# Optimization experiments

Measured on AMD Instinct MI355X. Metric: run time of the kernel, lower is better.

## Reference

```python
import jax, jax.numpy as jnp
import numpy as np

B = 131072
EPS = 1e-5

def _attn(x, Wq, Wk, Wv, Wo):
    # x: (B, 10, 1); Wq/Wk/Wv: (1, 16); Wo: (16, 1)
    Q = x @ Wq  # (B, 10, 16)
    K = x @ Wk
    V = x @ Wv
    A = jnp.einsum('bqd,bkd->bqk', Q, K) / 4.0  # sqrt(16) = 4
    A = jax.nn.softmax(A, axis=1)  # NOTE: torch Softmax(dim=1) -> axis 1, not -1
    out = jnp.einsum('bqk,bkd->bqd', A, V) @ Wo  # (B, 10, 1)
    return out[..., 0]  # squeeze -> (B, 10)

def _bn(h, gamma, beta):
    # BatchNorm1d training-mode math (batch stats, biased variance)
    mu = jnp.mean(h, axis=0)
    var = jnp.mean(jnp.square(h - mu), axis=0)
    return gamma * (h - mu) * jax.lax.rsqrt(var + EPS) + beta

def setup_inputs() -> dict:
    key = jax.random.key(0)
    ks = jax.random.split(key, 24)
    n = lambda k, shp, s=1.0: (jax.random.normal(k, shp, dtype=jnp.float32) * s)
    inp = {
        'x':   n(ks[0], (B, 10, 1)),
        'Wq1': n(ks[1], (1, 16)), 'Wk1': n(ks[2], (1, 16)),
        'Wv1': n(ks[3], (1, 16)), 'Wo1': n(ks[4], (16, 1)),
        'Wq2': n(ks[5], (1, 16)), 'Wk2': n(ks[6], (1, 16)),
        'Wv2': n(ks[7], (1, 16)), 'Wo2': n(ks[8], (16, 1)),
        # layer1: Linear(10,128) BN ReLU Linear(128,256) BN ReLU Linear(256,10)
        'W1a': n(ks[9], (10, 128), 0.3), 'b1a': jnp.zeros((128,), jnp.float32),
        'g1a': jnp.ones((128,), jnp.float32), 'be1a': jnp.zeros((128,), jnp.float32),
        'W1b': n(ks[10], (128, 256), 0.09), 'b1b': jnp.zeros((256,), jnp.float32),
        'g1b': jnp.ones((256,), jnp.float32), 'be1b': jnp.zeros((256,), jnp.float32),
        'W1c': n(ks[11], (256, 10), 0.06), 'b1c': jnp.zeros((10,), jnp.float32),
        # layer2: Linear(10,128) BN ReLU Linear(128,256) BN ReLU Linear(256,2)
        'W2a': n(ks[12], (10, 128), 0.3), 'b2a': jnp.zeros((128,), jnp.float32),
        'g2a': jnp.ones((128,), jnp.float32), 'be2a': jnp.zeros((128,), jnp.float32),
        'W2b': n(ks[13], (128, 256), 0.09), 'b2b': jnp.zeros((256,), jnp.float32),
        'g2b': jnp.ones((256,), jnp.float32), 'be2b': jnp.zeros((256,), jnp.float32),
        'W2c': n(ks[14], (256, 2), 0.06), 'b2c': jnp.zeros((2,), jnp.float32),
    }
    return inp

def reference(x, Wq1, Wk1, Wv1, Wo1, Wq2, Wk2, Wv2, Wo2,
              W1a, b1a, g1a, be1a, W1b, b1b, g1b, be1b, W1c, b1c,
              W2a, b2a, g2a, be2a, W2b, b2b, g2b, be2b, W2c, b2c):
    h = _attn(x, Wq1, Wk1, Wv1, Wo1)                 # (B, 10)
    h = jax.nn.relu(_bn(h @ W1a + b1a, g1a, be1a))   # (B, 128)
    h = jax.nn.relu(_bn(h @ W1b + b1b, g1b, be1b))   # (B, 256)
    h = h @ W1c + b1c                                # (B, 10)
    h = _attn(h[..., None], Wq2, Wk2, Wv2, Wo2)      # (B, 10)
    h = jax.nn.relu(_bn(h @ W2a + b2a, g2a, be2a))   # (B, 128)
    h = jax.nn.relu(_bn(h @ W2b + b2b, g2b, be2b))   # (B, 256)
    return h @ W2c + b2c                             # (B, 2)
```

## Files before the change

kernel.cpp:

```cpp
#include <hip/hip_runtime.h>
#include <hip/hip_bf16.h>

#define EPS 1e-5f
constexpr int BN = 131072;
constexpr int NBKT = 32;

typedef __attribute__((ext_vector_type(8))) short bf16x8;
typedef __attribute__((ext_vector_type(4))) float f32x4;

constexpr size_t OFF_H   = 0;
constexpr size_t OFF_HH  = OFF_H  + (size_t)BN*10;
constexpr size_t OFF_M1  = OFF_HH + (size_t)BN*10;
constexpr size_t OFF_S2  = OFF_M1 + 65;
constexpr size_t OFF_M3  = OFF_S2 + 512;
constexpr size_t OFF_S4  = OFF_M3 + 65;
constexpr size_t OFF_WA1 = OFF_S4 + 512;
constexpr size_t OFF_BA1 = OFF_WA1 + 1280;
constexpr size_t OFF_WA2 = OFF_BA1 + 128;
constexpr size_t OFF_BA2 = OFF_WA2 + 1280;
constexpr size_t OFF_SC2 = OFF_BA2 + 128;
constexpr size_t OFF_TC2 = OFF_SC2 + 256;
constexpr size_t OFF_SC4 = OFF_TC2 + 256;
constexpr size_t OFF_TC4 = OFF_SC4 + 256;
constexpr size_t OFF_WB1 = OFF_TC4 + 256;
constexpr size_t OFF_BB1 = OFF_WB1 + 32768;
constexpr size_t OFF_WB2 = OFF_BB1 + 256;
constexpr size_t OFF_BB2 = OFF_WB2 + 32768;
constexpr size_t OFF_P1  = OFF_BB2 + 256;
constexpr size_t OFF_P3  = OFF_P1 + 1024*65;
constexpr size_t OFF_S2B = OFF_P3 + 1024*65;
constexpr size_t OFF_S4B = OFF_S2B + (size_t)NBKT*512;
constexpr size_t OFF_WT1 = OFF_S4B + (size_t)NBKT*512;
constexpr size_t OFF_WT2 = OFF_WT1 + 16384;
constexpr size_t OFF_END = OFF_WT2 + 16384;
constexpr size_t OFF_Z_BYTES = ((OFF_END*4 + 255) & ~(size_t)255);
constexpr size_t WS_NEED = OFF_Z_BYTES + (size_t)256*BN*2;

__device__ __forceinline__ float wsum(float v){
  v += __shfl_down(v, 32);
  v += __shfl_down(v, 16);
  v += __shfl_down(v, 8);
  v += __shfl_down(v, 4);
  v += __shfl_down(v, 2);
  v += __shfl_down(v, 1);
  return v;
}

__device__ __forceinline__ unsigned pk_bf16(float a, float b){
  union { __hip_bfloat16 h[2]; unsigned u; } cv;
  cv.h[0] = __float2bfloat16(a);
  cv.h[1] = __float2bfloat16(b);
  return cv.u;
}

__device__ __forceinline__ unsigned short bf16_1(float a){
  union { __hip_bfloat16 h; unsigned short u; } cv;
  cv.h = __float2bfloat16(a);
  return cv.u;
}

__device__ __forceinline__ void attn10(const float* xr, float cqk, float cvo, float* y){
  #pragma unroll
  for (int q=0;q<10;q++) y[q] = 0.f;
  #pragma unroll
  for (int k=0;k<10;k++){
    float t = cqk * xr[k];
    float m = t*xr[0];
    #pragma unroll
    for (int q=1;q<10;q++) m = fmaxf(m, t*xr[q]);
    float ex[10]; float s = 0.f;
    #pragma unroll
    for (int q=0;q<10;q++){ ex[q] = __expf(t*xr[q]-m); s += ex[q]; }
    float f = xr[k]/s;
    #pragma unroll
    for (int q=0;q<10;q++) y[q] += ex[q]*f;
  }
  #pragma unroll
  for (int q=0;q<10;q++) y[q] *= cvo;
}

__device__ __forceinline__ void moments_block(const float* y, float (*red)[65],
                                              float* Pb, int t){
  int lane = t & 63, w = t >> 6;
  #pragma unroll
  for (int i=0;i<10;i++){
    float v = wsum(y[i]);
    if (lane==0) red[w][i] = v;
  }
  #pragma unroll
  for (int i=0;i<10;i++){
    #pragma unroll
    for (int j=i;j<10;j++){
      float v = wsum(y[i]*y[j]);
      if (lane==0) red[w][10 + 10*i - i*(i-1)/2 + (j-i)] = v;
    }
  }
  __syncthreads();
  if (t < 65)
    Pb[(size_t)blockIdx.x*65 + t] = red[0][t]+red[1][t]+red[2][t]+red[3][t];
}

__device__ __forceinline__ void moments10(const float* y, float* M, int lane){
  #pragma unroll
  for (int i=0;i<10;i++){
    float s = wsum(y[i]);
    if (lane==0) atomicAdd(&M[i], s);
  }
  #pragma unroll
  for (int i=0;i<10;i++){
    #pragma unroll
    for (int j=i;j<10;j++){
      int id = 10*i - i*(i-1)/2 + (j-i);
      float s = wsum(y[i]*y[j]);
      if (lane==0) atomicAdd(&M[10+id], s);
    }
  }
}

__global__ __launch_bounds__(256) void k_attn_in(
    const float* __restrict__ x,
    const float* __restrict__ Wq, const float* __restrict__ Wk,
    const float* __restrict__ Wv, const float* __restrict__ Wo,
    float* __restrict__ h, float* __restrict__ Pb){
  __shared__ float xs[256][11];
  __shared__ float red[4][65];
  int t = threadIdx.x;
  size_t base = (size_t)blockIdx.x*2560;
  for (int idx=t; idx<2560; idx+=256) xs[idx/10][idx%10] = x[base+idx];
  float cqk=0.f, cvo=0.f;
  #pragma unroll
  for (int d=0;d<16;d++){ cqk += Wq[d]*Wk[d]; cvo += Wv[d]*Wo[d]; }
  cqk *= 0.25f;
  __syncthreads();
  float xr[10];
  #pragma unroll
  for (int q=0;q<10;q++) xr[q] = xs[t][q];
  float y[10];
  attn10(xr, cqk, cvo, y);
  #pragma unroll
  for (int q=0;q<10;q++) xs[t][q] = y[q];
  moments_block(y, red, Pb, t);
  for (int idx=t; idx<2560; idx+=256) h[base+idx] = xs[idx/10][idx%10];
}

__global__ void k_fold10_part(const float* __restrict__ Pb, int npart,
                              const float* __restrict__ W,
                              const float* __restrict__ bv, const float* __restrict__ g,
                              const float* __restrict__ be,
                              float* __restrict__ WT, float* __restrict__ bo){
  __shared__ float part[65][8];
  __shared__ float sM[65];
  int t = threadIdx.x;
  if (t < 520){
    int c = t>>3, k = t&7;
    int n = npart>>3;
    float acc = 0.f;
    #pragma unroll 4
    for (int i=0;i<n;i++) acc += Pb[(size_t)(k*n+i)*65 + c];
    part[c][k] = acc;
  }
  __syncthreads();
  if (t < 65){
    float a = 0.f;
    #pragma unroll
    for (int k=0;k<8;k++) a += part[t][k];
    sM[t] = a;
  }
  __syncthreads();
  int j = t;
  if (j >= 128) return;
  const float invB = 1.f/(float)BN;
  float Eh[10];
  #pragma unroll
  for (int i=0;i<10;i++) Eh[i] = sM[i]*invB;
  float wj[10];
  #pragma unroll
  for (int i=0;i<10;i++) wj[i] = W[i*128+j];
  float mu = bv[j];
  #pragma unroll
  for (int i=0;i<10;i++) mu += Eh[i]*wj[i];
  float var = 0.f;
  #pragma unroll
  for (int i=0;i<10;i++){
    #pragma unroll
    for (int l=0;l<10;l++){
      int a = i<l ? i : l, c = i<l ? l : i;
      int id = 10*a - a*(a-1)/2 + (c-a);
      float cov = sM[10+id]*invB - Eh[i]*Eh[l];
      var += wj[i]*wj[l]*cov;
    }
  }
  float s = g[j]*rsqrtf(var + EPS);
  #pragma unroll
  for (int i=0;i<10;i++) WT[j*10+i] = wj[i]*s;
  bo[j] = (bv[j]-mu)*s + be[j];
}

__global__ void k_fold10_atomic(const float* __restrict__ M,
                                const float* __restrict__ W,
                                const float* __restrict__ bv, const float* __restrict__ g,
                                const float* __restrict__ be,
                                float* __restrict__ WT, float* __restrict__ bo){
  int j = threadIdx.x;
  if (j >= 128) return;
  const float invB = 1.f/(float)BN;
  float Eh[10];
  #pragma unroll
  for (int i=0;i<10;i++) Eh[i] = M[i]*invB;
  float wj[10];
  #pragma unroll
  for (int i=0;i<10;i++) wj[i] = W[i*128+j];
  float mu = bv[j];
  #pragma unroll
  for (int i=0;i<10;i++) mu += Eh[i]*wj[i];
  float var = 0.f;
  #pragma unroll
  for (int i=0;i<10;i++){
    #pragma unroll
    for (int l=0;l<10;l++){
      int a = i<l ? i : l, c = i<l ? l : i;
      int id = 10*a - a*(a-1)/2 + (c-a);
      float cov = M[10+id]*invB - Eh[i]*Eh[l];
      var += wj[i]*wj[l]*cov;
    }
  }
  float s = g[j]*rsqrtf(var + EPS);
  #pragma unroll
  for (int i=0;i<10;i++) WT[j*10+i] = wj[i]*s;
  bo[j] = (bv[j]-mu)*s + be[j];
}

__global__ void k_fold_affine(const float* __restrict__ stats,
                              const float* __restrict__ g,
                              const float* __restrict__ be,
                              float* __restrict__ s, float* __restrict__ tt){
  int j = threadIdx.x;
  if (j >= 256) return;
  float su = 0.f, sq = 0.f;
  #pragma unroll 4
  for (int k=0;k<NBKT;k++){
    su += stats[k*512 + j];
    sq += stats[k*512 + 256 + j];
  }
  const float invB = 1.f/(float)BN;
  float mu  = su*invB;
  float var = sq*invB - mu*mu;
  float sc = g[j]*rsqrtf(var + EPS);
  s[j]  = sc;
  tt[j] = be[j] - mu*sc;
}

__global__ __launch_bounds__(256) void k_prep_wt2(
    const float* __restrict__ W1, const float* __restrict__ W2,
    unsigned short* __restrict__ WT1, unsigned short* __restrict__ WT2){
  int g = blockIdx.x;
  const float* W = (g < 128) ? W1 : W2;
  unsigned short* WT = (g < 128) ? WT1 : WT2;
  int idx = (g & 127)*256 + threadIdx.x;
  int c = idx >> 7, k = idx & 127;
  WT[idx] = bf16_1(W[k*256 + c]);
}

__global__ __launch_bounds__(256) void k_layer_mfma(
    const float* __restrict__ h,
    const float* __restrict__ WaT,
    const float* __restrict__ ba,
    const unsigned short* __restrict__ WT,
    const float* __restrict__ bb,
    unsigned short* __restrict__ zt,
    float* __restrict__ stats)
{
  __shared__ unsigned short zs[256*72];
  __shared__ float hs[64][11];
  __shared__ float sWaT[1280];
  __shared__ float sstats[512];
  unsigned short* h1s = zs;
  int t = threadIdx.x;
  int lane = t & 63, w = t >> 6;
  int ci = lane & 15, g = lane >> 4;
  size_t row0 = (size_t)blockIdx.x * 64;

  bf16x8 bfr[4][4];
  #pragma unroll
  for (int nt=0; nt<4; nt++)
    #pragma unroll
    for (int kt=0; kt<4; kt++){
      union { uint4 u; bf16x8 v; } cv;
      cv.u = *(const uint4*)(WT + (size_t)(w*64 + nt*16 + ci)*128 + kt*32 + g*8);
      bfr[nt][kt] = cv.v;
    }

  for (int idx = t; idx < 640; idx += 256) hs[idx/10][idx%10] = h[row0*10 + idx];
  for (int idx = t; idx < 1280; idx += 256) sWaT[idx] = WaT[idx];
  __syncthreads();

  {
    int r = lane;
    int i0 = w * 32;
    float hr[10];
    #pragma unroll
    for (int l=0;l<10;l++) hr[l] = hs[r][l];
    #pragma unroll
    for (int j=0;j<4;j++){
      unsigned pk[4];
      #pragma unroll
      for (int q=0;q<4;q++){
        int i = i0 + j*8 + q*2;
        float v0 = ba[i], v1 = ba[i+1];
        #pragma unroll
        for (int l=0;l<10;l++){
          v0 = fmaf(hr[l], sWaT[i*10+l],     v0);
          v1 = fmaf(hr[l], sWaT[(i+1)*10+l], v1);
        }
        pk[q] = pk_bf16(fmaxf(v0,0.f), fmaxf(v1,0.f));
      }
      int byte = r*256 + (((i0 + j*8)*2) ^ ((r&7)<<4));
      *(uint4*)((char*)h1s + byte) = make_uint4(pk[0],pk[1],pk[2],pk[3]);
    }
  }
  __syncthreads();

  f32x4 acc[4][4];
  #pragma unroll
  for (int mt=0;mt<4;mt++)
    #pragma unroll
    for (int nt=0;nt<4;nt++)
      acc[mt][nt] = (f32x4){0.f,0.f,0.f,0.f};

  #pragma unroll
  for (int mt=0; mt<4; mt++){
    int r = mt*16 + ci;
    bf16x8 af[4];
    #pragma unroll
    for (int kt=0; kt<4; kt++){
      int byte = r*256 + ((kt*64 + g*16) ^ ((r&7)<<4));
      af[kt] = *(const bf16x8*)((const char*)h1s + byte);
    }
    #pragma unroll
    for (int nt=0; nt<4; nt++)
      #pragma unroll
      for (int kt=0; kt<4; kt++)
        acc[mt][nt] = __builtin_amdgcn_mfma_f32_16x16x32_bf16(
            af[kt], bfr[nt][kt], acc[mt][nt], 0, 0, 0);
  }

  float bbv[4];
  #pragma unroll
  for (int nt=0;nt<4;nt++) bbv[nt] = bb[w*64 + nt*16 + ci];
  float csum[4] = {0,0,0,0}, csq[4] = {0,0,0,0};
  #pragma unroll
  for (int mt=0; mt<4; mt++)
    #pragma unroll
    for (int nt=0; nt<4; nt++)
      #pragma unroll
      for (int j=0;j<4;j++){
        float zv = acc[mt][nt][j] + bbv[nt];
        acc[mt][nt][j] = zv;
        csum[nt] += zv;
        csq[nt]  += zv*zv;
      }
  #pragma unroll
  for (int nt=0; nt<4; nt++){
    float s1 = csum[nt], s2 = csq[nt];
    s1 += __shfl_down(s1, 32); s1 += __shfl_down(s1, 16);
    s2 += __shfl_down(s2, 32); s2 += __shfl_down(s2, 16);
    if (lane < 16){
      sstats[w*64 + nt*16 + ci]       = s1;
      sstats[256 + w*64 + nt*16 + ci] = s2;
    }
  }
  __syncthreads();
  int bkt = blockIdx.x & (NBKT-1);
  atomicAdd(&stats[bkt*512 + t], sstats[t]);
  atomicAdd(&stats[bkt*512 + 256 + t], sstats[256+t]);

  #pragma unroll
  for (int mt=0; mt<4; mt++)
    #pragma unroll
    for (int nt=0; nt<4; nt++){
      int c = w*64 + nt*16 + ci;
      int r0 = mt*16 + g*4;
      uint2 v;
      v.x = pk_bf16(acc[mt][nt][0], acc[mt][nt][1]);
      v.y = pk_bf16(acc[mt][nt][2], acc[mt][nt][3]);
      *(uint2*)&zs[c*72 + r0] = v;
    }
  __syncthreads();

  #pragma unroll
  for (int pass=0; pass<8; pass++){
    int c  = (t>>3) + pass*32;
    int rc = (t&7)*8;
    uint4 v = *(const uint4*)&zs[c*72 + rc];
    *(uint4*)(zt + (size_t)c*BN + row0 + rc) = v;
  }
}

__global__ __launch_bounds__(256) void k_consume_mid(
    const unsigned short* __restrict__ zt,
    const float* __restrict__ s_g, const float* __restrict__ t_g,
    const float* __restrict__ Wc,  const float* __restrict__ bc,
    const float* __restrict__ Wq, const float* __restrict__ Wk,
    const float* __restrict__ Wv, const float* __restrict__ Wo,
    float* __restrict__ hh, float* __restrict__ Pb){
  __shared__ __align__(16) unsigned short zs[64*256];
  __shared__ float sW[2560];
  __shared__ float ss[256], st[256];
  __shared__ float red[4][65];
  int t = threadIdx.x;
  for (int idx=t; idx<2560; idx+=256) sW[idx] = Wc[idx];
  ss[t] = s_g[t]; st[t] = t_g[t];
  size_t b0 = (size_t)blockIdx.x*256;

  float z3[10];
  #pragma unroll
  for (int l=0;l<10;l++) z3[l] = bc[l];

  int lane32 = t & 31, cl8 = t >> 5;
  for (int cc=0; cc<4; cc++){
    __syncthreads();
    #pragma unroll
    for (int pass=0; pass<8; pass++){
      int c_local = pass*8 + cl8;
      int c = cc*64 + c_local;
      uint4 v = *(const uint4*)(zt + (size_t)c*BN + b0 + lane32*8);
      *(uint4*)&zs[c_local*256 + lane32*8] = v;
    }
    __syncthreads();
    #pragma unroll 8
    for (int c_local=0; c_local<64; c_local++){
      int c = cc*64 + c_local;
      float f = __uint_as_float(((unsigned)zs[c_local*256 + t]) << 16);
      float h2 = fmaxf(fmaf(ss[c], f, st[c]), 0.f);
      #pragma unroll
      for (int l=0;l<10;l++) z3[l] = fmaf(h2, sW[c*10+l], z3[l]);
    }
  }

  float cqk=0.f, cvo=0.f;
  #pragma unroll
  for (int d=0;d<16;d++){ cqk += Wq[d]*Wk[d]; cvo += Wv[d]*Wo[d]; }
  cqk *= 0.25f;
  float y[10];
  attn10(z3, cqk, cvo, y);
  __syncthreads();
  float* hhs = (float*)zs;
  #pragma unroll
  for (int q=0;q<10;q++) hhs[t*10+q] = y[q];
  moments_block(y, red, Pb, t);
  for (int idx=t; idx<2560; idx+=256)
    hh[b0*10 + idx] = hhs[idx];
}

__global__ __launch_bounds__(256) void k_consume_out(
    const unsigned short* __restrict__ zt,
    const float* __restrict__ s_g, const float* __restrict__ t_g,
    const float* __restrict__ Wc,  const float* __restrict__ bc,
    float* __restrict__ out){
  __shared__ __align__(16) unsigned short zs[64*256];
  __shared__ float sW0[256], sW1[256], ss[256], st[256];
  int t = threadIdx.x;
  sW0[t] = Wc[t*2]; sW1[t] = Wc[t*2+1];
  ss[t] = s_g[t]; st[t] = t_g[t];
  size_t b0 = (size_t)blockIdx.x*256;
  float o0 = bc[0], o1 = bc[1];
  int lane32 = t & 31, cl8 = t >> 5;
  for (int cc=0; cc<4; cc++){
    __syncthreads();
    #pragma unroll
    for (int pass=0; pass<8; pass++){
      int c_local = pass*8 + cl8;
      int c = cc*64 + c_local;
      uint4 v = *(const uint4*)(zt + (size_t)c*BN + b0 + lane32*8);
      *(uint4*)&zs[c_local*256 + lane32*8] = v;
    }
    __syncthreads();
    #pragma unroll 8
    for (int c_local=0; c_local<64; c_local++){
      int c = cc*64 + c_local;
      float f = __uint_as_float(((unsigned)zs[c_local*256 + t]) << 16);
      float h5 = fmaxf(fmaf(ss[c], f, st[c]), 0.f);
      o0 = fmaf(h5, sW0[c], o0);
      o1 = fmaf(h5, sW1[c], o1);
    }
  }
  *(float2*)(out + (b0 + t)*2) = make_float2(o0, o1);
}

__global__ void k_fold_big(const float* __restrict__ stats,
                           const float* __restrict__ W,
                           const float* __restrict__ bv, const float* __restrict__ g,
                           const float* __restrict__ be,
                           float* __restrict__ Wf, float* __restrict__ bf){
  int j = blockIdx.x*256 + threadIdx.x;
  if (j >= 256) return;
  const float invB = 1.f/(float)BN;
  float mu  = stats[j]*invB;
  float var = stats[256+j]*invB - mu*mu;
  float s = g[j]*rsqrtf(var + EPS);
  bf[j] = (bv[j]-mu)*s + be[j];
  for (int i=0;i<128;i++) Wf[i*256+j] = W[i*256+j]*s;
}

__global__ __launch_bounds__(256) void k_mid(
    const float* __restrict__ h,
    const float* __restrict__ WaT, const float* __restrict__ ba,
    const float* __restrict__ Wb,  const float* __restrict__ bb,
    float* __restrict__ stats){
  int b = blockIdx.x*256 + threadIdx.x;
  if (b >= BN) return;
  float hr[10];
  #pragma unroll
  for (int l=0;l<10;l++) hr[l] = h[(size_t)b*10+l];
  int lane = threadIdx.x & 63;
  for (int jc=0;jc<4;jc++){
    float acc[64];
    #pragma unroll
    for (int j=0;j<64;j++) acc[j] = bb[jc*64+j];
    for (int i=0;i<128;i++){
      float h1 = ba[i];
      #pragma unroll
      for (int l=0;l<10;l++) h1 += hr[l]*WaT[i*10+l];
      h1 = fmaxf(h1, 0.f);
      const float* __restrict__ w = &Wb[i*256 + jc*64];
      #pragma unroll
      for (int j=0;j<64;j++) acc[j] += h1*w[j];
    }
    #pragma unroll
    for (int j=0;j<64;j++){
      float s1 = wsum(acc[j]);
      float s2 = wsum(acc[j]*acc[j]);
      if (lane==0){
        atomicAdd(&stats[jc*64+j], s1);
        atomicAdd(&stats[256+jc*64+j], s2);
      }
    }
  }
}

__global__ __launch_bounds__(256) void k_mid2(
    const float* __restrict__ h,
    const float* __restrict__ WaT, const float* __restrict__ ba,
    const float* __restrict__ Wbf, const float* __restrict__ bbf,
    const float* __restrict__ Wc,  const float* __restrict__ bc,
    const float* __restrict__ Wq, const float* __restrict__ Wk,
    const float* __restrict__ Wv, const float* __restrict__ Wo,
    float* __restrict__ hh, float* __restrict__ M){
  int b = blockIdx.x*256 + threadIdx.x;
  if (b >= BN) return;
  float hr[10];
  #pragma unroll
  for (int l=0;l<10;l++) hr[l] = h[(size_t)b*10+l];
  float z3[10];
  #pragma unroll
  for (int l=0;l<10;l++) z3[l] = bc[l];
  for (int jc=0;jc<4;jc++){
    float acc[64];
    #pragma unroll
    for (int j=0;j<64;j++) acc[j] = bbf[jc*64+j];
    for (int i=0;i<128;i++){
      float h1 = ba[i];
      #pragma unroll
      for (int l=0;l<10;l++) h1 += hr[l]*WaT[i*10+l];
      h1 = fmaxf(h1, 0.f);
      const float* __restrict__ w = &Wbf[i*256 + jc*64];
      #pragma unroll
      for (int j=0;j<64;j++) acc[j] += h1*w[j];
    }
    #pragma unroll
    for (int j=0;j<64;j++){
      float h2 = fmaxf(acc[j], 0.f);
      const float* __restrict__ wc = &Wc[(jc*64+j)*10];
      #pragma unroll
      for (int l=0;l<10;l++) z3[l] += h2*wc[l];
    }
  }
  float cqk=0.f, cvo=0.f;
  #pragma unroll
  for (int d=0;d<16;d++){ cqk += Wq[d]*Wk[d]; cvo += Wv[d]*Wo[d]; }
  cqk *= 0.25f;
  float y[10];
  attn10(z3, cqk, cvo, y);
  #pragma unroll
  for (int q=0;q<10;q++) hh[(size_t)b*10+q] = y[q];
  moments10(y, M, threadIdx.x & 63);
}

__global__ __launch_bounds__(256) void k_out(
    const float* __restrict__ h,
    const float* __restrict__ WaT, const float* __restrict__ ba,
    const float* __restrict__ Wbf, const float* __restrict__ bbf,
    const float* __restrict__ Wc,  const float* __restrict__ bc,
    float* __restrict__ out){
  int b = blockIdx.x*256 + threadIdx.x;
  if (b >= BN) return;
  float hr[10];
  #pragma unroll
  for (int l=0;l<10;l++) hr[l] = h[(size_t)b*10+l];
  float o0 = bc[0], o1 = bc[1];
  for (int jc=0;jc<4;jc++){
    float acc[64];
    #pragma unroll
    for (int j=0;j<64;j++) acc[j] = bbf[jc*64+j];
    for (int i=0;i<128;i++){
      float h4 = ba[i];
      #pragma unroll
      for (int l=0;l<10;l++) h4 += hr[l]*WaT[i*10+l];
      h4 = fmaxf(h4, 0.f);
      const float* __restrict__ w = &Wbf[i*256 + jc*64];
      #pragma unroll
      for (int j=0;j<64;j++) acc[j] += h4*w[j];
    }
    #pragma unroll
    for (int j=0;j<64;j++){
      float h5 = fmaxf(acc[j], 0.f);
      o0 += h5*Wc[(jc*64+j)*2];
      o1 += h5*Wc[(jc*64+j)*2+1];
    }
  }
  out[(size_t)b*2]   = o0;
  out[(size_t)b*2+1] = o1;
}

extern "C" void kernel_launch(void* const* d_in, const int* in_sizes, int n_in,
                              void* d_out, int out_size, void* d_ws, size_t ws_size,
                              hipStream_t stream){
  const float* x   = (const float*)d_in[0];
  const float* Wq1 = (const float*)d_in[1];
  const float* Wk1 = (const float*)d_in[2];
  const float* Wv1 = (const float*)d_in[3];
  const float* Wo1 = (const float*)d_in[4];
  const float* Wq2 = (const float*)d_in[5];
  const float* Wk2 = (const float*)d_in[6];
  const float* Wv2 = (const float*)d_in[7];
  const float* Wo2 = (const float*)d_in[8];
  const float* W1a = (const float*)d_in[9];  const float* b1a = (const float*)d_in[10];
  const float* g1a = (const float*)d_in[11]; const float* be1a= (const float*)d_in[12];
  const float* W1b = (const float*)d_in[13]; const float* b1b = (const float*)d_in[14];
  const float* g1b = (const float*)d_in[15]; const float* be1b= (const float*)d_in[16];
  const float* W1c = (const float*)d_in[17]; const float* b1c = (const float*)d_in[18];
  const float* W2a = (const float*)d_in[19]; const float* b2a = (const float*)d_in[20];
  const float* g2a = (const float*)d_in[21]; const float* be2a= (const float*)d_in[22];
  const float* W2b = (const float*)d_in[23]; const float* b2b = (const float*)d_in[24];
  const float* g2b = (const float*)d_in[25]; const float* be2b= (const float*)d_in[26];
  const float* W2c = (const float*)d_in[27]; const float* b2c = (const float*)d_in[28];

  float* f   = (float*)d_ws;
  float* h   = f + OFF_H;
  float* hh  = f + OFF_HH;
  float* M1  = f + OFF_M1;
  float* S2  = f + OFF_S2;
  float* M3  = f + OFF_M3;
  float* S4  = f + OFF_S4;
  float* WA1 = f + OFF_WA1; float* BA1 = f + OFF_BA1;
  float* WA2 = f + OFF_WA2; float* BA2 = f + OFF_BA2;
  float* SC2 = f + OFF_SC2; float* TC2 = f + OFF_TC2;
  float* SC4 = f + OFF_SC4; float* TC4 = f + OFF_TC4;
  float* WB1 = f + OFF_WB1; float* BB1 = f + OFF_BB1;
  float* WB2 = f + OFF_WB2; float* BB2 = f + OFF_BB2;
  float* P1  = f + OFF_P1;  float* P3  = f + OFF_P3;
  float* S2B = f + OFF_S2B; float* S4B = f + OFF_S4B;
  unsigned short* WT1 = (unsigned short*)(f + OFF_WT1);
  unsigned short* WT2 = (unsigned short*)(f + OFF_WT2);
  unsigned short* ZT = (unsigned short*)((char*)d_ws + OFF_Z_BYTES);

  dim3 blk(256);
  dim3 grid256(BN/256);
  dim3 grid64(BN/64);

  if (ws_size >= WS_NEED){
    hipMemsetAsync(S2B, 0, (size_t)2*NBKT*512*sizeof(float), stream);
    k_prep_wt2<<<256,blk,0,stream>>>(W1b, W2b, WT1, WT2);
    k_attn_in<<<grid256,blk,0,stream>>>(x, Wq1,Wk1,Wv1,Wo1, h, P1);
    k_fold10_part<<<1,576,0,stream>>>(P1, 512, W1a,b1a,g1a,be1a, WA1,BA1);
    k_layer_mfma<<<grid64,blk,0,stream>>>(h, WA1,BA1, WT1,b1b, ZT, S2B);
    k_fold_affine<<<1,256,0,stream>>>(S2B, g1b, be1b, SC2, TC2);
    k_consume_mid<<<grid256,blk,0,stream>>>(ZT, SC2,TC2, W1c,b1c,
                                            Wq2,Wk2,Wv2,Wo2, hh, P3);
    k_fold10_part<<<1,576,0,stream>>>(P3, 512, W2a,b2a,g2a,be2a, WA2,BA2);
    k_layer_mfma<<<grid64,blk,0,stream>>>(hh, WA2,BA2, WT2,b2b, ZT, S4B);
    k_fold_affine<<<1,256,0,stream>>>(S4B, g2b, be2b, SC4, TC4);
    k_consume_out<<<grid256,blk,0,stream>>>(ZT, SC4,TC4, W2c,b2c, (float*)d_out);
  } else {
    hipMemsetAsync(M1, 0, (65+512+65+512)*sizeof(float), stream);
    k_attn_in<<<grid256,blk,0,stream>>>(x, Wq1,Wk1,Wv1,Wo1, h, P1);
    k_fold10_part<<<1,576,0,stream>>>(P1, 512, W1a,b1a,g1a,be1a, WA1,BA1);
    k_mid<<<grid256,blk,0,stream>>>(h, WA1,BA1, W1b,b1b, S2);
    k_fold_big<<<1,256,0,stream>>>(S2, W1b,b1b,g1b,be1b, WB1,BB1);
    k_mid2<<<grid256,blk,0,stream>>>(h, WA1,BA1, WB1,BB1, W1c,b1c,
                                     Wq2,Wk2,Wv2,Wo2, hh, M3);
    k_fold10_atomic<<<1,128,0,stream>>>(M3, W2a,b2a,g2a,be2a, WA2,BA2);
    k_mid<<<grid256,blk,0,stream>>>(hh, WA2,BA2, W2b,b2b, S4);
    k_fold_big<<<1,256,0,stream>>>(S4, W2b,b2b,g2b,be2b, WB2,BB2);
    k_out<<<grid256,blk,0,stream>>>(hh, WA2,BA2, WB2,BB2, W2c,b2c, (float*)d_out);
  }
}
```

Measured before the change: 209.9 us.

## Recompute 128x256 GEMM instead of materializing bf16 activations to HBM

```diff
diff --git a/kernel.cpp b/kernel.cpp
--- a/kernel.cpp
+++ b/kernel.cpp
@@ -27,14 +27,13 @@
 constexpr size_t OFF_WB2 = OFF_BB1 + 256;
 constexpr size_t OFF_BB2 = OFF_WB2 + 32768;
 constexpr size_t OFF_P1  = OFF_BB2 + 256;
-constexpr size_t OFF_P3  = OFF_P1 + 1024*65;
-constexpr size_t OFF_S2B = OFF_P3 + 1024*65;
+constexpr size_t OFF_P3  = OFF_P1 + 2048*65;
+constexpr size_t OFF_S2B = OFF_P3 + 2048*65;
 constexpr size_t OFF_S4B = OFF_S2B + (size_t)NBKT*512;
 constexpr size_t OFF_WT1 = OFF_S4B + (size_t)NBKT*512;
 constexpr size_t OFF_WT2 = OFF_WT1 + 16384;
 constexpr size_t OFF_END = OFF_WT2 + 16384;
-constexpr size_t OFF_Z_BYTES = ((OFF_END*4 + 255) & ~(size_t)255);
-constexpr size_t WS_NEED = OFF_Z_BYTES + (size_t)256*BN*2;
+constexpr size_t WS_NEED = OFF_END*4;
 
 __device__ __forceinline__ float wsum(float v){
   v += __shfl_down(v, 32);
@@ -231,6 +230,7 @@
 }
 
 __global__ void k_fold_affine(const float* __restrict__ stats,
+                              const float* __restrict__ bb,
                               const float* __restrict__ g,
                               const float* __restrict__ be,
                               float* __restrict__ s, float* __restrict__ tt){
@@ -247,7 +247,7 @@
   float var = sq*invB - mu*mu;
   float sc = g[j]*rsqrtf(var + EPS);
   s[j]  = sc;
-  tt[j] = be[j] - mu*sc;
+  tt[j] = be[j] - mu*sc + sc*bb[j];
 }
 
 __global__ __launch_bounds__(256) void k_prep_wt2(
@@ -261,24 +261,14 @@
   WT[idx] = bf16_1(W[k*256 + c]);
 }
 
-__global__ __launch_bounds__(256) void k_layer_mfma(
-    const float* __restrict__ h,
-    const float* __restrict__ WaT,
-    const float* __restrict__ ba,
-    const unsigned short* __restrict__ WT,
-    const float* __restrict__ bb,
-    unsigned short* __restrict__ zt,
-    float* __restrict__ stats)
+__device__ __forceinline__ void block_gemm(
+    const float* __restrict__ h, const float* __restrict__ WaT,
+    const float* __restrict__ ba, const unsigned short* __restrict__ WT,
+    unsigned short* h1s, float (*hs)[11], float* sWaT,
+    f32x4 (&acc)[4][4], int t, size_t row0)
 {
-  __shared__ unsigned short zs[256*72];
-  __shared__ float hs[64][11];
-  __shared__ float sWaT[1280];
-  __shared__ float sstats[512];
-  unsigned short* h1s = zs;
-  int t = threadIdx.x;
   int lane = t & 63, w = t >> 6;
   int ci = lane & 15, g = lane >> 4;
-  size_t row0 = (size_t)blockIdx.x * 64;
 
   bf16x8 bfr[4][4];
   #pragma unroll
@@ -320,7 +310,6 @@
   }
   __syncthreads();
 
-  f32x4 acc[4][4];
   #pragma unroll
   for (int mt=0;mt<4;mt++)
     #pragma unroll
@@ -343,6 +332,24 @@
         acc[mt][nt] = __builtin_amdgcn_mfma_f32_16x16x32_bf16(
             af[kt], bfr[nt][kt], acc[mt][nt], 0, 0, 0);
   }
+}
+
+__global__ __launch_bounds__(256) void k_stats(
+    const float* __restrict__ h, const float* __restrict__ WaT,
+    const float* __restrict__ ba, const unsigned short* __restrict__ WT,
+    const float* __restrict__ bb, float* __restrict__ stats)
+{
+  __shared__ unsigned short h1s[64*128];
+  __shared__ float hs[64][11];
+  __shared__ float sWaT[1280];
+  __shared__ float sstats[512];
+  int t = threadIdx.x;
+  int lane = t & 63, w = t >> 6;
+  int ci = lane & 15;
+  size_t row0 = (size_t)blockIdx.x * 64;
+
+  f32x4 acc[4][4];
+  block_gemm(h, WaT, ba, WT, h1s, hs, sWaT, acc, t, row0);
 
   float bbv[4];
   #pragma unroll
@@ -355,7 +362,6 @@
       #pragma unroll
       for (int j=0;j<4;j++){
         float zv = acc[mt][nt][j] + bbv[nt];
-        acc[mt][nt][j] = zv;
         csum[nt] += zv;
         csq[nt]  += zv*zv;
       }
@@ -373,118 +379,166 @@
   int bkt = blockIdx.x & (NBKT-1);
   atomicAdd(&stats[bkt*512 + t], sstats[t]);
   atomicAdd(&stats[bkt*512 + 256 + t], sstats[256+t]);
-
-  #pragma unroll
-  for (int mt=0; mt<4; mt++)
-    #pragma unroll
-    for (int nt=0; nt<4; nt++){
-      int c = w*64 + nt*16 + ci;
-      int r0 = mt*16 + g*4;
-      uint2 v;
-      v.x = pk_bf16(acc[mt][nt][0], acc[mt][nt][1]);
-      v.y = pk_bf16(acc[mt][nt][2], acc[mt][nt][3]);
-      *(uint2*)&zs[c*72 + r0] = v;
-    }
-  __syncthreads();
-
-  #pragma unroll
-  for (int pass=0; pass<8; pass++){
-    int c  = (t>>3) + pass*32;
-    int rc = (t&7)*8;
-    uint4 v = *(const uint4*)&zs[c*72 + rc];
-    *(uint4*)(zt + (size_t)c*BN + row0 + rc) = v;
-  }
-}
-
-__global__ __launch_bounds__(256) void k_consume_mid(
-    const unsigned short* __restrict__ zt,
+}
+
+__global__ __launch_bounds__(256) void k_fuse_mid(
+    const float* __restrict__ h, const float* __restrict__ WaT,
+    const float* __restrict__ ba, const unsigned short* __restrict__ WT,
     const float* __restrict__ s_g, const float* __restrict__ t_g,
     const float* __restrict__ Wc,  const float* __restrict__ bc,
     const float* __restrict__ Wq, const float* __restrict__ Wk,
     const float* __restrict__ Wv, const float* __restrict__ Wo,
-    float* __restrict__ hh, float* __restrict__ Pb){
-  __shared__ __align__(16) unsigned short zs[64*256];
-  __shared__ float sW[2560];
-  __shared__ float ss[256], st[256];
-  __shared__ float red[4][65];
+    float* __restrict__ hh, float* __restrict__ Pb)
+{
+  __shared__ unsigned short h1s[64*128];
+  __shared__ float hs[64][11];
+  __shared__ float sWaT[1280];
+  __shared__ float sWc[2560];
+  __shared__ float ssv[256], stv[256];
+  __shared__ float z3part[4][64][10];
+  __shared__ float red[65];
+  __shared__ float hhs[64][10];
   int t = threadIdx.x;
-  for (int idx=t; idx<2560; idx+=256) sW[idx] = Wc[idx];
-  ss[t] = s_g[t]; st[t] = t_g[t];
-  size_t b0 = (size_t)blockIdx.x*256;
-
-  float z3[10];
-  #pragma unroll
-  for (int l=0;l<10;l++) z3[l] = bc[l];
-
-  int lane32 = t & 31, cl8 = t >> 5;
-  for (int cc=0; cc<4; cc++){
-    __syncthreads();
-    #pragma unroll
-    for (int pass=0; pass<8; pass++){
-      int c_local = pass*8 + cl8;
-      int c = cc*64 + c_local;
-      uint4 v = *(const uint4*)(zt + (size_t)c*BN + b0 + lane32*8);
-      *(uint4*)&zs[c_local*256 + lane32*8] = v;
-    }
-    __syncthreads();
-    #pragma unroll 8
-    for (int c_local=0; c_local<64; c_local++){
-      int c = cc*64 + c_local;
-      float f = __uint_as_float(((unsigned)zs[c_local*256 + t]) << 16);
-      float h2 = fmaxf(fmaf(ss[c], f, st[c]), 0.f);
-      #pragma unroll
-      for (int l=0;l<10;l++) z3[l] = fmaf(h2, sW[c*10+l], z3[l]);
-    }
-  }
+  int lane = t & 63, w = t >> 6;
+  int ci = lane & 15, g = lane >> 4;
+  size_t row0 = (size_t)blockIdx.x * 64;
+
+  for (int idx=t; idx<2560; idx+=256) sWc[idx] = Wc[idx];
+  ssv[t] = s_g[t]; stv[t] = t_g[t];
+
+  f32x4 acc[4][4];
+  block_gemm(h, WaT, ba, WT, h1s, hs, sWaT, acc, t, row0);
+
+  float sv[4], tv[4], wcv[4][10];
+  #pragma unroll
+  for (int nt=0;nt<4;nt++){
+    int c = w*64 + nt*16 + ci;
+    sv[nt] = ssv[c]; tv[nt] = stv[c];
+    #pragma unroll
+    for (int l=0;l<10;l++) wcv[nt][l] = sWc[c*10+l];
+  }
+
+  #pragma unroll
+  for (int mt=0; mt<4; mt++){
+    #pragma unroll
+    for (int j=0;j<4;j++){
+      float p[10];
+      #pragma unroll
+      for (int l=0;l<10;l++) p[l] = 0.f;
+      #pragma unroll
+      for (int nt=0;nt<4;nt++){
+        float h2 = fmaxf(fmaf(sv[nt], acc[mt][nt][j], tv[nt]), 0.f);
+        #pragma unroll
+        for (int l=0;l<10;l++) p[l] = fmaf(h2, wcv[nt][l], p[l]);
+      }
+      #pragma unroll
+      for (int off=1; off<16; off<<=1){
+        #pragma unroll
+        for (int l=0;l<10;l++) p[l] += __shfl_xor(p[l], off);
+      }
+      if (ci==0){
+        int row = mt*16 + g*4 + j;
+        #pragma unroll
+        for (int l=0;l<10;l++) z3part[w][row][l] = p[l];
+      }
+    }
+  }
+  __syncthreads();
 
   float cqk=0.f, cvo=0.f;
   #pragma unroll
   for (int d=0;d<16;d++){ cqk += Wq[d]*Wk[d]; cvo += Wv[d]*Wo[d]; }
   cqk *= 0.25f;
+
   float y[10];
-  attn10(z3, cqk, cvo, y);
-  __syncthreads();
-  float* hhs = (float*)zs;
-  #pragma unroll
-  for (int q=0;q<10;q++) hhs[t*10+q] = y[q];
-  moments_block(y, red, Pb, t);
-  for (int idx=t; idx<2560; idx+=256)
-    hh[b0*10 + idx] = hhs[idx];
-}
-
-__global__ __launch_bounds__(256) void k_consume_out(
-    const unsigned short* __restrict__ zt,
+  if (t < 64){
+    float z3[10];
+    #pragma unroll
+    for (int l=0;l<10;l++)
+      z3[l] = bc[l] + z3part[0][t][l] + z3part[1][t][l]
+                    + z3part[2][t][l] + z3part[3][t][l];
+    attn10(z3, cqk, cvo, y);
+    #pragma unroll
+    for (int q=0;q<10;q++) hhs[t][q] = y[q];
+    #pragma unroll
+    for (int i=0;i<10;i++){
+      float v = wsum(y[i]);
+      if (lane==0) red[i] = v;
+    }
+    #pragma unroll
+    for (int i=0;i<10;i++){
+      #pragma unroll
+      for (int j=i;j<10;j++){
+        float v = wsum(y[i]*y[j]);
+        if (lane==0) red[10 + 10*i - i*(i-1)/2 + (j-i)] = v;
+      }
+    }
+  }
+  __syncthreads();
+  if (t < 65) Pb[(size_t)blockIdx.x*65 + t] = red[t];
+  const float* hhsf = (const float*)hhs;
+  for (int idx=t; idx<640; idx+=256) hh[row0*10 + idx] = hhsf[idx];
+}
+
+__global__ __launch_bounds__(256) void k_fuse_out(
+    const float* __restrict__ h, const float* __restrict__ WaT,
+    const float* __restrict__ ba, const unsigned short* __restrict__ WT,
     const float* __restrict__ s_g, const float* __restrict__ t_g,
     const float* __restrict__ Wc,  const float* __restrict__ bc,
-    float* __restrict__ out){
-  __shared__ __align__(16) unsigned short zs[64*256];
-  __shared__ float sW0[256], sW1[256], ss[256], st[256];
+    float* __restrict__ out)
+{
+  __shared__ unsigned short h1s[64*128];
+  __shared__ float hs[64][11];
+  __shared__ float sWaT[1280];
+  __shared__ float sW0[256], sW1[256], ssv[256], stv[256];
+  __shared__ float opart[4][64][2];
   int t = threadIdx.x;
+  int lane = t & 63, w = t >> 6;
+  int ci = lane & 15, g = lane >> 4;
+  size_t row0 = (size_t)blockIdx.x * 64;
+
   sW0[t] = Wc[t*2]; sW1[t] = Wc[t*2+1];
-  ss[t] = s_g[t]; st[t] = t_g[t];
-  size_t b0 = (size_t)blockIdx.x*256;
-  float o0 = bc[0], o1 = bc[1];
-  int lane32 = t & 31, cl8 = t >> 5;
-  for (int cc=0; cc<4; cc++){
-    __syncthreads();
-    #pragma unroll
-    for (int pass=0; pass<8; pass++){
-      int c_local = pass*8 + cl8;
-      int c = cc*64 + c_local;
-      uint4 v = *(const uint4*)(zt + (size_t)c*BN + b0 + lane32*8);
-      *(uint4*)&zs[c_local*256 + lane32*8] = v;
-    }
-    __syncthreads();
-    #pragma unroll 8
-    for (int c_local=0; c_local<64; c_local++){
-      int c = cc*64 + c_local;
-      float f = __uint_as_float(((unsigned)zs[c_local*256 + t]) << 16);
-      float h5 = fmaxf(fmaf(ss[c], f, st[c]), 0.f);
-      o0 = fmaf(h5, sW0[c], o0);
-      o1 = fmaf(h5, sW1[c], o1);
-    }
-  }
-  *(float2*)(out + (b0 + t)*2) = make_float2(o0, o1);
+  ssv[t] = s_g[t];  stv[t] = t_g[t];
+
+  f32x4 acc[4][4];
+  block_gemm(h, WaT, ba, WT, h1s, hs, sWaT, acc, t, row0);
+
+  float sv[4], tv[4], w0[4], w1[4];
+  #pragma unroll
+  for (int nt=0;nt<4;nt++){
+    int c = w*64 + nt*16 + ci;
+    sv[nt] = ssv[c]; tv[nt] = stv[c];
+    w0[nt] = sW0[c]; w1[nt] = sW1[c];
+  }
+  #pragma unroll
+  for (int mt=0; mt<4; mt++){
+    #pragma unroll
+    for (int j=0;j<4;j++){
+      float p0 = 0.f, p1 = 0.f;
+      #pragma unroll
+      for (int nt=0;nt<4;nt++){
+        float h5 = fmaxf(fmaf(sv[nt], acc[mt][nt][j], tv[nt]), 0.f);
+        p0 = fmaf(h5, w0[nt], p0);
+        p1 = fmaf(h5, w1[nt], p1);
+      }
+      #pragma unroll
+      for (int off=1; off<16; off<<=1){
+        p0 += __shfl_xor(p0, off);
+        p1 += __shfl_xor(p1, off);
+      }
+      if (ci==0){
+        int row = mt*16 + g*4 + j;
+        opart[w][row][0] = p0;
+        opart[w][row][1] = p1;
+      }
+    }
+  }
+  __syncthreads();
+  if (t < 64){
+    float o0 = bc[0] + opart[0][t][0]+opart[1][t][0]+opart[2][t][0]+opart[3][t][0];
+    float o1 = bc[1] + opart[0][t][1]+opart[1][t][1]+opart[2][t][1]+opart[3][t][1];
+    *(float2*)(out + (row0 + t)*2) = make_float2(o0, o1);
+  }
 }
 
 __global__ void k_fold_big(const float* __restrict__ stats,
@@ -662,7 +716,6 @@
   float* S2B = f + OFF_S2B; float* S4B = f + OFF_S4B;
   unsigned short* WT1 = (unsigned short*)(f + OFF_WT1);
   unsigned short* WT2 = (unsigned short*)(f + OFF_WT2);
-  unsigned short* ZT = (unsigned short*)((char*)d_ws + OFF_Z_BYTES);
 
   dim3 blk(256);
   dim3 grid256(BN/256);
@@ -673,14 +726,15 @@
     k_prep_wt2<<<256,blk,0,stream>>>(W1b, W2b, WT1, WT2);
     k_attn_in<<<grid256,blk,0,stream>>>(x, Wq1,Wk1,Wv1,Wo1, h, P1);
     k_fold10_part<<<1,576,0,stream>>>(P1, 512, W1a,b1a,g1a,be1a, WA1,BA1);
-    k_layer_mfma<<<grid64,blk,0,stream>>>(h, WA1,BA1, WT1,b1b, ZT, S2B);
-    k_fold_affine<<<1,256,0,stream>>>(S2B, g1b, be1b, SC2, TC2);
-    k_consume_mid<<<grid256,blk,0,stream>>>(ZT, SC2,TC2, W1c,b1c,
-                                            Wq2,Wk2,Wv2,Wo2, hh, P3);
-    k_fold10_part<<<1,576,0,stream>>>(P3, 512, W2a,b2a,g2a,be2a, WA2,BA2);
-    k_layer_mfma<<<grid64,blk,0,stream>>>(hh, WA2,BA2, WT2,b2b, ZT, S4B);
-    k_fold_affine<<<1,256,0,stream>>>(S4B, g2b, be2b, SC4, TC4);
-    k_consume_out<<<grid256,blk,0,stream>>>(ZT, SC4,TC4, W2c,b2c, (float*)d_out);
+    k_stats<<<grid64,blk,0,stream>>>(h, WA1,BA1, WT1, b1b, S2B);
+    k_fold_affine<<<1,256,0,stream>>>(S2B, b1b, g1b, be1b, SC2, TC2);
+    k_fuse_mid<<<grid64,blk,0,stream>>>(h, WA1,BA1, WT1, SC2,TC2, W1c,b1c,
+                                        Wq2,Wk2,Wv2,Wo2, hh, P3);
+    k_fold10_part<<<1,576,0,stream>>>(P3, 2048, W2a,b2a,g2a,be2a, WA2,BA2);
+    k_stats<<<grid64,blk,0,stream>>>(hh, WA2,BA2, WT2, b2b, S4B);
+    k_fold_affine<<<1,256,0,stream>>>(S4B, b2b, g2b, be2b, SC4, TC4);
+    k_fuse_out<<<grid64,blk,0,stream>>>(hh, WA2,BA2, WT2, SC4,TC4,
+                                        W2c,b2c, (float*)d_out);
   } else {
     hipMemsetAsync(M1, 0, (65+512+65+512)*sizeof(float), stream);
     k_attn_in<<<grid256,blk,0,stream>>>(x, Wq1,Wk1,Wv1,Wo1, h, P1);
```

Result: slower. 336.3 us (+60.2%).

## Shrink LDS footprint, vectorize weight reads, and defer stats atomics

Applied to the files above, without the earlier changes.

```diff
diff --git a/kernel.cpp b/kernel.cpp
--- a/kernel.cpp
+++ b/kernel.cpp
@@ -59,6 +59,10 @@
   return cv.u;
 }
 
+__device__ __forceinline__ float bf16_to_f(unsigned short u){
+  return __uint_as_float(((unsigned)u) << 16);
+}
+
 __device__ __forceinline__ void attn10(const float* xr, float cqk, float cvo, float* y){
   #pragma unroll
   for (int q=0;q<10;q++) y[q] = 0.f;
@@ -261,24 +265,14 @@
   WT[idx] = bf16_1(W[k*256 + c]);
 }
 
-__global__ __launch_bounds__(256) void k_layer_mfma(
-    const float* __restrict__ h,
-    const float* __restrict__ WaT,
-    const float* __restrict__ ba,
-    const unsigned short* __restrict__ WT,
-    const float* __restrict__ bb,
-    unsigned short* __restrict__ zt,
-    float* __restrict__ stats)
+__device__ __forceinline__ void block_gemm(
+    const float* __restrict__ h, const float* __restrict__ WaT,
+    const float* __restrict__ ba, const unsigned short* __restrict__ WT,
+    unsigned short* h1s, float (*hs)[11], float* sWaT,
+    f32x4 (&acc)[4][4], int t, size_t row0)
 {
-  __shared__ unsigned short zs[256*72];
-  __shared__ float hs[64][11];
-  __shared__ float sWaT[1280];
-  __shared__ float sstats[512];
-  unsigned short* h1s = zs;
-  int t = threadIdx.x;
   int lane = t & 63, w = t >> 6;
   int ci = lane & 15, g = lane >> 4;
-  size_t row0 = (size_t)blockIdx.x * 64;
 
   bf16x8 bfr[4][4];
   #pragma unroll
@@ -320,7 +314,6 @@
   }
   __syncthreads();
 
-  f32x4 acc[4][4];
   #pragma unroll
   for (int mt=0;mt<4;mt++)
     #pragma unroll
@@ -343,36 +336,51 @@
         acc[mt][nt] = __builtin_amdgcn_mfma_f32_16x16x32_bf16(
             af[kt], bfr[nt][kt], acc[mt][nt], 0, 0, 0);
   }
+}
+
+__global__ __launch_bounds__(256) void k_layer_mfma(
+    const float* __restrict__ h,
+    const float* __restrict__ WaT,
+    const float* __restrict__ ba,
+    const unsigned short* __restrict__ WT,
+    const float* __restrict__ bb,
+    unsigned short* __restrict__ zt,
+    float* __restrict__ stats)
+{
+  __shared__ __align__(16) char smem[36864];
+  unsigned short* h1s = (unsigned short*)smem;
+  float (*hs)[11]     = (float(*)[11])(smem + 16384);
+  float* sWaT         = (float*)(smem + 19200);
+  unsigned short* zs  = (unsigned short*)smem;
+  int t = threadIdx.x;
+  int lane = t & 63, w = t >> 6;
+  int ci = lane & 15, g = lane >> 4;
+  size_t row0 = (size_t)blockIdx.x * 64;
+
+  f32x4 acc[4][4];
+  block_gemm(h, WaT, ba, WT, h1s, hs, sWaT, acc, t, row0);
 
   float bbv[4];
   #pragma unroll
   for (int nt=0;nt<4;nt++) bbv[nt] = bb[w*64 + nt*16 + ci];
-  float csum[4] = {0,0,0,0}, csq[4] = {0,0,0,0};
-  #pragma unroll
-  for (int mt=0; mt<4; mt++)
-    #pragma unroll
-    for (int nt=0; nt<4; nt++)
+  float s1v[4], s2v[4];
+  #pragma unroll
+  for (int nt=0; nt<4; nt++){
+    float cs = 0.f, cq = 0.f;
+    #pragma unroll
+    for (int mt=0; mt<4; mt++)
       #pragma unroll
       for (int j=0;j<4;j++){
         float zv = acc[mt][nt][j] + bbv[nt];
         acc[mt][nt][j] = zv;
-        csum[nt] += zv;
-        csq[nt]  += zv*zv;
+        cs += zv;
+        cq += zv*zv;
       }
-  #pragma unroll
-  for (int nt=0; nt<4; nt++){
-    float s1 = csum[nt], s2 = csq[nt];
-    s1 += __shfl_down(s1, 32); s1 += __shfl_down(s1, 16);
-    s2 += __shfl_down(s2, 32); s2 += __shfl_down(s2, 16);
-    if (lane < 16){
-      sstats[w*64 + nt*16 + ci]       = s1;
-      sstats[256 + w*64 + nt*16 + ci] = s2;
-    }
-  }
-  __syncthreads();
-  int bkt = blockIdx.x & (NBKT-1);
-  atomicAdd(&stats[bkt*512 + t], sstats[t]);
-  atomicAdd(&stats[bkt*512 + 256 + t], sstats[256+t]);
+    cs += __shfl_down(cs, 32); cs += __shfl_down(cs, 16);
+    cq += __shfl_down(cq, 32); cq += __shfl_down(cq, 16);
+    s1v[nt] = cs; s2v[nt] = cq;
+  }
+  __syncthreads();
 
   #pragma unroll
   for (int mt=0; mt<4; mt++)
@@ -394,6 +402,16 @@
     uint4 v = *(const uint4*)&zs[c*72 + rc];
     *(uint4*)(zt + (size_t)c*BN + row0 + rc) = v;
   }
+
+  if (lane < 16){
+    int bkt = blockIdx.x & (NBKT-1);
+    #pragma unroll
+    for (int nt=0; nt<4; nt++){
+      int c = w*64 + nt*16 + ci;
+      atomicAdd(&stats[bkt*512 + c],       s1v[nt]);
+      atomicAdd(&stats[bkt*512 + 256 + c], s2v[nt]);
+    }
+  }
 }
 
 __global__ __launch_bounds__(256) void k_consume_mid(
@@ -403,12 +421,12 @@
     const float* __restrict__ Wq, const float* __restrict__ Wk,
     const float* __restrict__ Wv, const float* __restrict__ Wo,
     float* __restrict__ hh, float* __restrict__ Pb){
-  __shared__ __align__(16) unsigned short zs[64*256];
-  __shared__ float sW[2560];
+  __shared__ __align__(16) unsigned short zs[32*256];
+  __shared__ __align__(16) float sWc[256*12];
   __shared__ float ss[256], st[256];
   __shared__ float red[4][65];
   int t = threadIdx.x;
-  for (int idx=t; idx<2560; idx+=256) sW[idx] = Wc[idx];
+  for (int idx=t; idx<2560; idx+=256) sWc[(idx/10)*12 + (idx%10)] = Wc[idx];
   ss[t] = s_g[t]; st[t] = t_g[t];
   size_t b0 = (size_t)blockIdx.x*256;
 
@@ -416,24 +434,30 @@
   #pragma unroll
   for (int l=0;l<10;l++) z3[l] = bc[l];
 
-  int lane32 = t & 31, cl8 = t >> 5;
-  for (int cc=0; cc<4; cc++){
+  int c8 = t >> 3, i8 = t & 7;
+  for (int cc=0; cc<8; cc++){
     __syncthreads();
-    #pragma unroll
-    for (int pass=0; pass<8; pass++){
-      int c_local = pass*8 + cl8;
-      int c = cc*64 + c_local;
-      uint4 v = *(const uint4*)(zt + (size_t)c*BN + b0 + lane32*8);
-      *(uint4*)&zs[c_local*256 + lane32*8] = v;
+    {
+      int c = cc*32 + c8;
+      const uint4* src = (const uint4*)(zt + (size_t)c*BN + b0 + i8*32);
+      uint4* dst = (uint4*)&zs[c8*256 + i8*32];
+      dst[0] = src[0]; dst[1] = src[1]; dst[2] = src[2]; dst[3] = src[3];
     }
     __syncthreads();
-    #pragma unroll 8
-    for (int c_local=0; c_local<64; c_local++){
-      int c = cc*64 + c_local;
-      float f = __uint_as_float(((unsigned)zs[c_local*256 + t]) << 16);
+    #pragma unroll 4
+    for (int cl=0; cl<32; cl++){
+      int c = cc*32 + cl;
+      float f = bf16_to_f(zs[cl*256 + t]);
       float h2 = fmaxf(fmaf(ss[c], f, st[c]), 0.f);
-      #pragma unroll
-      for (int l=0;l<10;l++) z3[l] = fmaf(h2, sW[c*10+l], z3[l]);
+      const float4* wr = (const float4*)&sWc[c*12];
+      float4 w0 = wr[0];
+      float4 w1 = wr[1];
+      float2 w2 = *(const float2*)&sWc[c*12 + 8];
+      z3[0] = fmaf(h2, w0.x, z3[0]); z3[1] = fmaf(h2, w0.y, z3[1]);
+      z3[2] = fmaf(h2, w0.z, z3[2]); z3[3] = fmaf(h2, w0.w, z3[3]);
+      z3[4] = fmaf(h2, w1.x, z3[4]); z3[5] = fmaf(h2, w1.y, z3[5]);
+      z3[6] = fmaf(h2, w1.z, z3[6]); z3[7] = fmaf(h2, w1.w, z3[7]);
+      z3[8] = fmaf(h2, w2.x, z3[8]); z3[9] = fmaf(h2, w2.y, z3[9]);
     }
   }
 
@@ -457,31 +481,32 @@
     const float* __restrict__ s_g, const float* __restrict__ t_g,
     const float* __restrict__ Wc,  const float* __restrict__ bc,
     float* __restrict__ out){
-  __shared__ __align__(16) unsigned short zs[64*256];
-  __shared__ float sW0[256], sW1[256], ss[256], st[256];
+  __shared__ __align__(16) unsigned short zs[32*256];
+  __shared__ __align__(8) float sWo[512];
+  __shared__ float ss[256], st[256];
   int t = threadIdx.x;
-  sW0[t] = Wc[t*2]; sW1[t] = Wc[t*2+1];
+  sWo[t] = Wc[t]; sWo[256+t] = Wc[256+t];
   ss[t] = s_g[t]; st[t] = t_g[t];
   size_t b0 = (size_t)blockIdx.x*256;
   float o0 = bc[0], o1 = bc[1];
-  int lane32 = t & 31, cl8 = t >> 5;
-  for (int cc=0; cc<4; cc++){
+  int c8 = t >> 3, i8 = t & 7;
+  for (int cc=0; cc<8; cc++){
     __syncthreads();
-    #pragma unroll
-    for (int pass=0; pass<8; pass++){
-      int c_local = pass*8 + cl8;
-      int c = cc*64 + c_local;
-      uint4 v = *(const uint4*)(zt + (size_t)c*BN + b0 + lane32*8);
-      *(uint4*)&zs[c_local*256 + lane32*8] = v;
+    {
+      int c = cc*32 + c8;
+      const uint4* src = (const uint4*)(zt + (size_t)c*BN + b0 + i8*32);
+      uint4* dst = (uint4*)&zs[c8*256 + i8*32];
+      dst[0] = src[0]; dst[1] = src[1]; dst[2] = src[2]; dst[3] = src[3];
     }
     __syncthreads();
     #pragma unroll 8
-    for (int c_local=0; c_local<64; c_local++){
-      int c = cc*64 + c_local;
-      float f = __uint_as_float(((unsigned)zs[c_local*256 + t]) << 16);
+    for (int cl=0; cl<32; cl++){
+      int c = cc*32 + cl;
+      float f = bf16_to_f(zs[cl*256 + t]);
       float h5 = fmaxf(fmaf(ss[c], f, st[c]), 0.f);
-      o0 = fmaf(h5, sW0[c], o0);
-      o1 = fmaf(h5, sW1[c], o1);
+      float2 wv = *(const float2*)&sWo[c*2];
+      o0 = fmaf(h5, wv.x, o0);
+      o1 = fmaf(h5, wv.y, o1);
     }
   }
   *(float2*)(out + (b0 + t)*2) = make_float2(o0, o1);
```

Result: slower. 218.5 us (+4.1%).
